# Performance work log

Measured on AMD Instinct MI355X. Metric: run time of the kernel, lower is better.

Reference implementation:

```python
import jax, jax.numpy as jnp
import numpy as np

NUM_HEADS = 16
HEAD_DIM = 128
ROTARY_DIM = 32  # head_dim * rotary_pct(0.25)
ROPE_BASE = 10000.0
SCALE = HEAD_DIM ** -0.5


def _rotate_half(x):
    x1, x2 = jnp.split(x, 2, axis=-1)
    return jnp.concatenate((-x2, x1), axis=-1)


def _rope_tables(seq_len, dtype):
    inv_freq = 1.0 / (ROPE_BASE ** (jnp.arange(0, ROTARY_DIM, 2, dtype=jnp.float32) / ROTARY_DIM))
    freqs = jnp.arange(seq_len, dtype=jnp.float32)[:, None] * inv_freq[None, :]  # [S, rd/2]
    emb = jnp.concatenate((freqs, freqs), axis=-1)  # [S, rd]
    return jnp.cos(emb).astype(dtype), jnp.sin(emb).astype(dtype)


def setup_inputs() -> dict:
    key = jax.random.key(0)
    k1, k2, k3 = jax.random.split(key, 3)
    B, S, H = 2, 2048, 2048
    hidden_states = jax.random.normal(k1, (B, S, H), dtype=jnp.float32)
    attention_mask = jnp.zeros((B, 1, S, S), dtype=jnp.float32)
    Wqkv = jax.random.normal(k2, (H, 3 * H), dtype=jnp.float32) * (H ** -0.5)
    Wout = jax.random.normal(k3, (H, H), dtype=jnp.float32) * (H ** -0.5)
    return {"hidden_states": hidden_states, "attention_mask": attention_mask,
            "Wqkv": Wqkv, "Wout": Wout}


def reference(hidden_states, attention_mask, Wqkv, Wout):
    B, S, H = hidden_states.shape
    qkv = jnp.einsum('bsh,hk->bsk', hidden_states, Wqkv)  # [B,S,3H]
    q, k, v = jnp.split(qkv, 3, axis=-1)

    def to_heads(x):
        return x.reshape(B, S, NUM_HEADS, HEAD_DIM).transpose(0, 2, 1, 3)  # [B,nh,S,hd]

    q, k, v = to_heads(q), to_heads(k), to_heads(v)

    cos, sin = _rope_tables(S, hidden_states.dtype)  # [S, ROTARY_DIM]
    cos = cos[None, None, :, :]
    sin = sin[None, None, :, :]

    def rope(x):
        xr = x[..., :ROTARY_DIM]
        xr = xr * cos + _rotate_half(xr) * sin
        return jnp.concatenate((xr, x[..., ROTARY_DIM:]), axis=-1)

    q, k = rope(q), rope(k)

    scores = jnp.einsum('bhqd,bhkd->bhqk', q, k) * SCALE + attention_mask
    probs = jax.nn.softmax(scores, axis=-1)  # dropout p=0 -> identity
    ctx = jnp.einsum('bhqk,bhkd->bhqd', probs, v)
    ctx = ctx.transpose(0, 2, 1, 3).reshape(B, S, H)
    return jnp.einsum('bsh,ho->bso', ctx, Wout)
```

## Files before the change

### kernel.cpp

```cpp
#include <hip/hip_runtime.h>

typedef __attribute__((ext_vector_type(4))) float f32x4;
typedef __attribute__((ext_vector_type(8))) short s16x8;
typedef __attribute__((ext_vector_type(4))) unsigned short u16x4;
typedef __attribute__((ext_vector_type(8))) unsigned short u16x8;

#define DEVINL __device__ __forceinline__

constexpr int Bb = 2;
constexpr int Ss = 2048;
constexpr int Hh = 2048;
constexpr int NH = 16;
constexpr int HD = 128;
constexpr float ATT_SCALE = 0.08838834764831845f;
constexpr float CEXP = ATT_SCALE * 1.44269504089f;
constexpr float INV_SCALE = 11.313708498984761f;
constexpr float RAW_THR = 90.50966799f;

DEVINL unsigned short f2bf(float f) {
    unsigned u = __float_as_uint(f);
    u += 0x7FFFu + ((u >> 16) & 1u);
    return (unsigned short)(u >> 16);
}
DEVINL float bf2f(unsigned short h) { return __uint_as_float(((unsigned)h) << 16); }
DEVINL float fexp2(float x) { return __builtin_amdgcn_exp2f(x); }

DEVINL void gl16(const void* g, void* l) {
    __builtin_amdgcn_global_load_lds((const __attribute__((address_space(1))) void*)g,
                                     (__attribute__((address_space(3))) void*)l, 16, 0, 0);
}

__global__ void scan_mask_k(const float* __restrict__ m, int* __restrict__ flag) {
    size_t i = ((size_t)blockIdx.x * 256 + threadIdx.x) * 4;
    f32x4 v = *(const f32x4*)(m + i);
    int any = (v[0] != 0.f) || (v[1] != 0.f) || (v[2] != 0.f) || (v[3] != 0.f);
    if (__any(any)) { if ((threadIdx.x & 63) == 0) atomicOr(flag, 1); }
}

__global__ void convH_k(const float* __restrict__ x, unsigned short* __restrict__ y) {
    size_t i = (size_t)blockIdx.x * 256 + threadIdx.x;
    f32x4 a = *(const f32x4*)(x + i * 8);
    f32x4 b = *(const f32x4*)(x + i * 8 + 4);
    u16x8 o;
    o[0] = f2bf(a[0]); o[1] = f2bf(a[1]); o[2] = f2bf(a[2]); o[3] = f2bf(a[3]);
    o[4] = f2bf(b[0]); o[5] = f2bf(b[1]); o[6] = f2bf(b[2]); o[7] = f2bf(b[3]);
    *(u16x8*)(y + i * 8) = o;
}

__global__ void convT_k(const float* __restrict__ W, unsigned short* __restrict__ Wt,
                        int R, int C) {
    __shared__ float tile[32][33];
    int c0 = blockIdx.x * 32, r0 = blockIdx.y * 32;
    int t = threadIdx.x;
    int rr = t >> 3, cc = (t & 7) * 4;
    f32x4 v = *(const f32x4*)(W + (size_t)(r0 + rr) * C + c0 + cc);
    tile[rr][cc + 0] = v[0]; tile[rr][cc + 1] = v[1];
    tile[rr][cc + 2] = v[2]; tile[rr][cc + 3] = v[3];
    __syncthreads();
    u16x4 o;
    o[0] = f2bf(tile[cc + 0][rr]); o[1] = f2bf(tile[cc + 1][rr]);
    o[2] = f2bf(tile[cc + 2][rr]); o[3] = f2bf(tile[cc + 3][rr]);
    *(u16x4*)(Wt + (size_t)(c0 + rr) * R + r0 + cc) = o;
}

template<int MODE>
__global__ __launch_bounds__(512, 2)
void gemm128x256_k(const unsigned short* __restrict__ A, const unsigned short* __restrict__ Bt,
                   float* __restrict__ Cf, unsigned short* __restrict__ Cb,
                   unsigned short* __restrict__ VtOut,
                   int M, int N, int K, int rm, int rn, int snx) {
    __shared__ char lds[98304];
    int t = threadIdx.x, w = t >> 6, ln = t & 63, lr = ln & 15, lg = ln >> 4;
    int wm = w >> 2, wn = w & 3;
    int f = blockIdx.x;
    int xcd = f & 7, i0 = f >> 3;
    int mb = (xcd / snx) * rm + i0 % rm;
    int nb = (xcd % snx) * rn + i0 / rm;
    int m0 = mb * 128, n0 = nb * 256;
    const char* Ab = (const char*)A;
    const char* Bbp = (const char*)Bt;

    f32x4 acc[4][4];
#pragma unroll
    for (int i = 0; i < 4; ++i)
#pragma unroll
        for (int j = 0; j < 4; ++j) { acc[i][j][0] = 0.f; acc[i][j][1] = 0.f; acc[i][j][2] = 0.f; acc[i][j][3] = 0.f; }

    auto STGA = [&](int sbuf, int skh, int kt) {
        int row = t >> 2, c = t & 3;
        int cs = c ^ ((row >> 1) & 3);
        gl16(Ab + ((size_t)(m0 + row) * K + kt * 64 + skh * 32) * 2 + cs * 16,
             lds + sbuf * 49152 + skh * 8192 + t * 16);
    };
    auto STGB = [&](int sbuf, int skh, int kt) {
#pragma unroll
        for (int rr = 0; rr < 2; ++rr) {
            int ci = rr * 512 + t;
            int row = ci >> 2, c = ci & 3;
            int cs = c ^ ((row >> 1) & 3);
            gl16(Bbp + ((size_t)(n0 + row) * K + kt * 64 + skh * 32) * 2 + cs * 16,
                 lds + sbuf * 49152 + 16384 + skh * 16384 + ci * 16);
        }
    };

#define PH128(buf, kh, sbuf, skh, st)                                             \
  {                                                                               \
    const char* Ap = lds + (buf) * 49152 + (kh) * 8192;                           \
    const char* Bp = lds + (buf) * 49152 + 16384 + (kh) * 16384;                  \
    s16x8 af[4], bfr[4];                                                          \
    _Pragma("unroll")                                                             \
    for (int i = 0; i < 4; ++i) {                                                 \
      int row = wm * 64 + i * 16 + lr;                                            \
      af[i] = *(const s16x8*)(Ap + row * 64 + ((lg ^ ((row >> 1) & 3)) * 16));    \
    }                                                                             \
    _Pragma("unroll")                                                             \
    for (int j = 0; j < 4; ++j) {                                                 \
      int row = wn * 64 + j * 16 + lr;                                            \
      bfr[j] = *(const s16x8*)(Bp + row * 64 + ((lg ^ ((row >> 1) & 3)) * 16));   \
    }                                                                             \
    STGA(sbuf, skh, st); STGB(sbuf, skh, st);                                     \
    __builtin_amdgcn_s_barrier();                                                 \
    asm volatile("s_waitcnt lgkmcnt(0)" ::: "memory");                            \
    __builtin_amdgcn_s_setprio(1);                                                \
    _Pragma("unroll")                                                             \
    for (int i = 0; i < 4; ++i)                                                   \
      _Pragma("unroll")                                                           \
      for (int j = 0; j < 4; ++j)                                                 \
        acc[i][j] = __builtin_amdgcn_mfma_f32_16x16x32_bf16(af[i], bfr[j],        \
                                                            acc[i][j], 0, 0, 0); \
    __builtin_amdgcn_s_setprio(0);                                                \
    asm volatile("s_waitcnt vmcnt(6)" ::: "memory");                              \
    __builtin_amdgcn_s_barrier();                                                 \
  }

    const int NT = K >> 6;
    STGA(0, 0, 0); STGB(0, 0, 0);
    STGA(0, 1, 0); STGB(0, 1, 0);
    STGA(1, 0, 1); STGB(1, 0, 1);
    asm volatile("s_waitcnt vmcnt(3)" ::: "memory");
    __builtin_amdgcn_s_barrier();

    for (int it = 0; it < (NT >> 1); ++it) {
        int e = it * 2;
        int e2 = (e + 2 < NT) ? e + 2 : e;
        int e3 = (e + 3 < NT) ? e + 3 : e + 1;
        PH128(0, 0,  1, 1, e + 1)
        PH128(0, 1,  0, 0, e2)
        PH128(1, 0,  0, 1, e2)
        PH128(1, 1,  1, 0, e3)
    }
    asm volatile("s_waitcnt vmcnt(0)" ::: "memory");
#undef PH128

    if (MODE == 0 && n0 >= 4096) {
#pragma unroll
        for (int i = 0; i < 4; ++i)
#pragma unroll
            for (int j = 0; j < 4; ++j) {
                int vcol = n0 - 4096 + wn * 64 + j * 16 + lr;
                int h = vcol >> 7, d = vcol & 127;
                int gr = m0 + wm * 64 + i * 16 + lg * 4;
                int bb = gr >> 11, si = gr & 2047;
                u16x4 o;
                o[0] = f2bf(acc[i][j][0]); o[1] = f2bf(acc[i][j][1]);
                o[2] = f2bf(acc[i][j][2]); o[3] = f2bf(acc[i][j][3]);
                *(u16x4*)(VtOut + ((size_t)(bb * 16 + h) * 128 + d) * 2048 + si) = o;
            }
        return;
    }

    if (MODE == 0 && (wn & 1) == 0) {
        float invf = fexp2((float)lr * -0.83048202372f);
#pragma unroll
        for (int i = 0; i < 4; ++i)
#pragma unroll
            for (int r = 0; r < 4; ++r) {
                int srow = (m0 + wm * 64 + i * 16 + lg * 4 + r) & (Ss - 1);
                float sn, cs;
                sincosf((float)srow * invf, &sn, &cs);
                float x1 = acc[i][0][r], x2 = acc[i][1][r];
                acc[i][0][r] = x1 * cs - x2 * sn;
                acc[i][1][r] = x2 * cs + x1 * sn;
            }
    }

#pragma unroll
    for (int i = 0; i < 4; ++i)
#pragma unroll
        for (int j = 0; j < 4; ++j)
#pragma unroll
            for (int r = 0; r < 4; ++r) {
                int gr = m0 + wm * 64 + i * 16 + lg * 4 + r;
                int gc = n0 + wn * 64 + j * 16 + lr;
                float vv = acc[i][j][r];
                if (MODE == 1) Cf[(size_t)gr * N + gc] = vv;
                else           Cb[(size_t)gr * N + gc] = f2bf(vv);
            }
}

__global__ __launch_bounds__(512)
void attn_k(const unsigned short* __restrict__ qkv, const unsigned short* __restrict__ Vt,
            const float* __restrict__ mask, unsigned short* __restrict__ ctxb,
            const int* __restrict__ flag) {
    __shared__ char ldsK[2][16384];
    __shared__ char ldsV[2][16384];
    __shared__ unsigned short ldsP[8][1024];
    int f = blockIdx.x;
    int swzb = (f & 7) * 64 + (f >> 3);
    int bh = swzb >> 4, qt = swzb & 15;
    int b = bh >> 4, h = bh & 15;
    int t = threadIdx.x, w = t >> 6, ln = t & 63, lr = ln & 15, lg = ln >> 4;
    int useMask = *flag;
    int qw0 = qt * 128 + w * 16;
    const char* qkvB = (const char*)qkv;
    const char* VtB = (const char*)Vt;

    auto STAGE = [&](int buf, int kk0s) {
#pragma unroll
        for (int c = 0; c < 2; ++c) {
            int ci = c * 512 + t;
            int krow = ci >> 4, kcb = (ci & 15) << 4;
            gl16(qkvB + (((size_t)(b * Ss + kk0s + krow)) * 6144 + 2048 + h * 128) * 2 + (kcb ^ ((krow & 7) << 4)),
                 ldsK[buf] + ci * 16);
            int vrow = ci >> 3, vcb = (ci & 7) << 4;
            gl16(VtB + (((size_t)(bh * 128 + vrow)) * 2048 + kk0s) * 2 + (vcb ^ ((vrow & 7) << 4)),
                 ldsV[buf] + ci * 16);
        }
    };

    s16x8 qf[4];
    size_t qbase = ((size_t)(b * Ss + qw0 + lr)) * 6144 + h * 128;
#pragma unroll
    for (int kc = 0; kc < 4; ++kc) qf[kc] = *(const s16x8*)(qkv + qbase + kc * 32 + lg * 8);

    float mr = -3e38f, lsum = 0.f;
    f32x4 ctxa[8];
#pragma unroll
    for (int dn = 0; dn < 8; ++dn) { ctxa[dn][0] = 0.f; ctxa[dn][1] = 0.f; ctxa[dn][2] = 0.f; ctxa[dn][3] = 0.f; }
    const float* mrow = mask + (size_t)b * Ss * Ss;

    STAGE(0, 0);
    asm volatile("s_waitcnt vmcnt(0)" ::: "memory");
    __builtin_amdgcn_s_barrier();

    for (int tix = 0; tix < 32; ++tix) {
        int kk0 = tix * 64;
        int cur = tix & 1;
        if (kk0 + 64 < Ss) STAGE(cur ^ 1, kk0 + 64);

        f32x4 st[4];
#pragma unroll
        for (int n = 0; n < 4; ++n) {
            f32x4 sacc = {0.f, 0.f, 0.f, 0.f};
            const char* kb = ldsK[cur] + (n * 16 + lr) * 256;
            int sw = (lr & 7) << 4;
            s16x8 kf0 = *(const s16x8*)(kb + ((0 * 64 + lg * 16) ^ sw));
            s16x8 kf1 = *(const s16x8*)(kb + ((1 * 64 + lg * 16) ^ sw));
            s16x8 kf2 = *(const s16x8*)(kb + ((2 * 64 + lg * 16) ^ sw));
            s16x8 kf3 = *(const s16x8*)(kb + ((3 * 64 + lg * 16) ^ sw));
            __builtin_amdgcn_s_setprio(1);
            sacc = __builtin_amdgcn_mfma_f32_16x16x32_bf16(kf0, qf[0], sacc, 0, 0, 0);
            sacc = __builtin_amdgcn_mfma_f32_16x16x32_bf16(kf1, qf[1], sacc, 0, 0, 0);
            sacc = __builtin_amdgcn_mfma_f32_16x16x32_bf16(kf2, qf[2], sacc, 0, 0, 0);
            sacc = __builtin_amdgcn_mfma_f32_16x16x32_bf16(kf3, qf[3], sacc, 0, 0, 0);
            __builtin_amdgcn_s_setprio(0);
            st[n] = sacc;
        }
        if (useMask) {
#pragma unroll
            for (int n = 0; n < 4; ++n)
#pragma unroll
                for (int r = 0; r < 4; ++r)
                    st[n][r] += mrow[(size_t)(qw0 + lr) * Ss + kk0 + n * 16 + lg * 4 + r] * INV_SCALE;
        }
        float pmax = st[0][0];
#pragma unroll
        for (int n = 0; n < 4; ++n)
#pragma unroll
            for (int r = 0; r < 4; ++r) pmax = fmaxf(pmax, st[n][r]);
        pmax = fmaxf(pmax, __shfl_xor(pmax, 16));
        pmax = fmaxf(pmax, __shfl_xor(pmax, 32));
        bool need = pmax > mr + RAW_THR;
        if (__any(need)) {
            float mn = fmaxf(mr, pmax);
            float al = fexp2((mr - mn) * CEXP);
            mr = mn;
            lsum *= al;
            float a0 = __shfl(al, lg * 4 + 0), a1 = __shfl(al, lg * 4 + 1);
            float a2 = __shfl(al, lg * 4 + 2), a3 = __shfl(al, lg * 4 + 3);
#pragma unroll
            for (int dn = 0; dn < 8; ++dn) {
                ctxa[dn][0] *= a0; ctxa[dn][1] *= a1; ctxa[dn][2] *= a2; ctxa[dn][3] *= a3;
            }
        }
        float mC = mr * CEXP;
        float rs = 0.f;
        u16x4 pk[4];
#pragma unroll
        for (int n = 0; n < 4; ++n)
#pragma unroll
            for (int r = 0; r < 4; ++r) {
                float p = fexp2(st[n][r] * CEXP - mC);
                rs += p;
                pk[n][r] = f2bf(p);
            }
        rs += __shfl_xor(rs, 16);
        rs += __shfl_xor(rs, 32);
        lsum += rs;
        char* pw = (char*)ldsP[w];
        int swp = (lr & 7) << 4;
#pragma unroll
        for (int n = 0; n < 4; ++n)
            *(u16x4*)(pw + lr * 128 + ((32 * n + 8 * lg) ^ swp)) = pk[n];
        asm volatile("s_waitcnt lgkmcnt(0)" ::: "memory");
        s16x8 pa[2];
#pragma unroll
        for (int c2 = 0; c2 < 2; ++c2)
            pa[c2] = *(const s16x8*)(pw + lr * 128 + ((64 * c2 + 16 * lg) ^ swp));
#pragma unroll
        for (int dn = 0; dn < 8; ++dn) {
            const char* vb = ldsV[cur] + (dn * 16 + lr) * 128;
            s16x8 vf0 = *(const s16x8*)(vb + ((0 * 64 + lg * 16) ^ swp));
            s16x8 vf1 = *(const s16x8*)(vb + ((1 * 64 + lg * 16) ^ swp));
            __builtin_amdgcn_s_setprio(1);
            ctxa[dn] = __builtin_amdgcn_mfma_f32_16x16x32_bf16(pa[0], vf0, ctxa[dn], 0, 0, 0);
            ctxa[dn] = __builtin_amdgcn_mfma_f32_16x16x32_bf16(pa[1], vf1, ctxa[dn], 0, 0, 0);
            __builtin_amdgcn_s_setprio(0);
        }
        asm volatile("s_waitcnt vmcnt(0)" ::: "memory");
        __builtin_amdgcn_s_barrier();
    }
    float l0 = 1.f / __shfl(lsum, lg * 4 + 0), l1 = 1.f / __shfl(lsum, lg * 4 + 1);
    float l2 = 1.f / __shfl(lsum, lg * 4 + 2), l3 = 1.f / __shfl(lsum, lg * 4 + 3);
#pragma unroll
    for (int dn = 0; dn < 8; ++dn) {
        size_t base = ((size_t)(b * Ss + qw0)) * Hh + h * 128 + dn * 16 + lr;
        ctxb[base + (size_t)(lg * 4 + 0) * Hh] = f2bf(ctxa[dn][0] * l0);
        ctxb[base + (size_t)(lg * 4 + 1) * Hh] = f2bf(ctxa[dn][1] * l1);
        ctxb[base + (size_t)(lg * 4 + 2) * Hh] = f2bf(ctxa[dn][2] * l2);
        ctxb[base + (size_t)(lg * 4 + 3) * Hh] = f2bf(ctxa[dn][3] * l3);
    }
}

extern "C" void kernel_launch(void* const* d_in, const int* in_sizes, int n_in,
                              void* d_out, int out_size, void* d_ws, size_t ws_size,
                              hipStream_t stream) {
    (void)in_sizes; (void)n_in; (void)out_size; (void)ws_size;
    const float* hidden = (const float*)d_in[0];
    const float* mask   = (const float*)d_in[1];
    const float* Wqkv   = (const float*)d_in[2];
    const float* Wout   = (const float*)d_in[3];
    float* out = (float*)d_out;

    char* ws = (char*)d_ws;
    size_t off = 0;
    auto alloc = [&](size_t bytes) { char* p = ws + off; off += (bytes + 255) & ~(size_t)255; return p; };
    unsigned short* hbf   = (unsigned short*)alloc((size_t)8388608 * 2);
    unsigned short* wqkvT = (unsigned short*)alloc((size_t)12582912 * 2);
    unsigned short* woutT = (unsigned short*)alloc((size_t)4194304 * 2);
    unsigned short* qkv   = (unsigned short*)alloc((size_t)25165824 * 2);
    unsigned short* Vt    = (unsigned short*)alloc((size_t)8388608 * 2);
    int* flag             = (int*)alloc(256);
    unsigned short* ctx = hbf;

    hipMemsetAsync(flag, 0, 4, stream);
    scan_mask_k<<<8192, 256, 0, stream>>>(mask, flag);
    convH_k<<<4096, 256, 0, stream>>>(hidden, hbf);
    convT_k<<<dim3(192, 64), 256, 0, stream>>>(Wqkv, wqkvT, 2048, 6144);
    convT_k<<<dim3(64, 64), 256, 0, stream>>>(Wout, woutT, 2048, 2048);
    gemm128x256_k<0><<<768, 512, 0, stream>>>(hbf, wqkvT, nullptr, qkv, Vt,
                                              4096, 6144, 2048, 16, 6, 4);
    attn_k<<<512, 512, 0, stream>>>(qkv, Vt, mask, ctx, flag);
    gemm128x256_k<1><<<256, 512, 0, stream>>>(ctx, woutT, out, nullptr, nullptr,
                                              4096, 2048, 2048, 16, 2, 4);
}
```

Before: 300.8 us.

## Rewrite attention kernel with 32x32 MFMA tiles and 4-wave blocks

The attention kernel switches from 16x16x32 to 32x32x16 bf16 MFMA, with each wave owning 32 query rows. Blocks go from 8 waves to 4, with launch bounds allowing 3 blocks per CU. K/V staging drops from double-buffered prefetch to a single buffer loaded synchronously each iteration. Larger MFMA tiles raise data reuse per LDS fragment load and cut shuffle work in softmax, but the loss of prefetch overlap may expose global load latency.

After: 416.5 us. 38.5% more time.

```diff
diff --git a/kernel.cpp b/kernel.cpp
--- a/kernel.cpp
+++ b/kernel.cpp
@@ -1,6 +1,7 @@
 #include <hip/hip_runtime.h>
 
 typedef __attribute__((ext_vector_type(4))) float f32x4;
+typedef __attribute__((ext_vector_type(16))) float f32x16;
 typedef __attribute__((ext_vector_type(8))) short s16x8;
 typedef __attribute__((ext_vector_type(4))) unsigned short u16x4;
 typedef __attribute__((ext_vector_type(8))) unsigned short u16x8;
@@ -198,87 +199,88 @@
             }
 }
 
-__global__ __launch_bounds__(512)
+__global__ __launch_bounds__(256, 3)
 void attn_k(const unsigned short* __restrict__ qkv, const unsigned short* __restrict__ Vt,
             const float* __restrict__ mask, unsigned short* __restrict__ ctxb,
             const int* __restrict__ flag) {
-    __shared__ char ldsK[2][16384];
-    __shared__ char ldsV[2][16384];
-    __shared__ unsigned short ldsP[8][1024];
+    __shared__ char ldsK[16384];
+    __shared__ char ldsV[16384];
+    __shared__ unsigned short ldsP[4][2048];
     int f = blockIdx.x;
     int swzb = (f & 7) * 64 + (f >> 3);
     int bh = swzb >> 4, qt = swzb & 15;
     int b = bh >> 4, h = bh & 15;
-    int t = threadIdx.x, w = t >> 6, ln = t & 63, lr = ln & 15, lg = ln >> 4;
+    int t = threadIdx.x, w = t >> 6, ln = t & 63;
+    int q5 = ln & 31, lg5 = ln >> 5;
     int useMask = *flag;
-    int qw0 = qt * 128 + w * 16;
+    int qb = qt * 128 + w * 32;
     const char* qkvB = (const char*)qkv;
     const char* VtB = (const char*)Vt;
 
-    auto STAGE = [&](int buf, int kk0s) {
-#pragma unroll
-        for (int c = 0; c < 2; ++c) {
-            int ci = c * 512 + t;
-            int krow = ci >> 4, kcb = (ci & 15) << 4;
-            gl16(qkvB + (((size_t)(b * Ss + kk0s + krow)) * 6144 + 2048 + h * 128) * 2 + (kcb ^ ((krow & 7) << 4)),
-                 ldsK[buf] + ci * 16);
-            int vrow = ci >> 3, vcb = (ci & 7) << 4;
-            gl16(VtB + (((size_t)(bh * 128 + vrow)) * 2048 + kk0s) * 2 + (vcb ^ ((vrow & 7) << 4)),
-                 ldsV[buf] + ci * 16);
-        }
-    };
-
-    s16x8 qf[4];
-    size_t qbase = ((size_t)(b * Ss + qw0 + lr)) * 6144 + h * 128;
-#pragma unroll
-    for (int kc = 0; kc < 4; ++kc) qf[kc] = *(const s16x8*)(qkv + qbase + kc * 32 + lg * 8);
+    s16x8 qf[8];
+    size_t qrow = ((size_t)(b * Ss + qb + q5)) * 6144 + h * 128;
+#pragma unroll
+    for (int dc = 0; dc < 8; ++dc) qf[dc] = *(const s16x8*)(qkv + qrow + dc * 16 + lg5 * 8);
 
     float mr = -3e38f, lsum = 0.f;
-    f32x4 ctxa[8];
-#pragma unroll
-    for (int dn = 0; dn < 8; ++dn) { ctxa[dn][0] = 0.f; ctxa[dn][1] = 0.f; ctxa[dn][2] = 0.f; ctxa[dn][3] = 0.f; }
+    f32x16 ctx[4];
+#pragma unroll
+    for (int dt = 0; dt < 4; ++dt)
+#pragma unroll
+        for (int r = 0; r < 16; ++r) ctx[dt][r] = 0.f;
     const float* mrow = mask + (size_t)b * Ss * Ss;
-
-    STAGE(0, 0);
-    asm volatile("s_waitcnt vmcnt(0)" ::: "memory");
-    __builtin_amdgcn_s_barrier();
 
     for (int tix = 0; tix < 32; ++tix) {
         int kk0 = tix * 64;
-        int cur = tix & 1;
-        if (kk0 + 64 < Ss) STAGE(cur ^ 1, kk0 + 64);
-
-        f32x4 st[4];
-#pragma unroll
-        for (int n = 0; n < 4; ++n) {
-            f32x4 sacc = {0.f, 0.f, 0.f, 0.f};
-            const char* kb = ldsK[cur] + (n * 16 + lr) * 256;
-            int sw = (lr & 7) << 4;
-            s16x8 kf0 = *(const s16x8*)(kb + ((0 * 64 + lg * 16) ^ sw));
-            s16x8 kf1 = *(const s16x8*)(kb + ((1 * 64 + lg * 16) ^ sw));
-            s16x8 kf2 = *(const s16x8*)(kb + ((2 * 64 + lg * 16) ^ sw));
-            s16x8 kf3 = *(const s16x8*)(kb + ((3 * 64 + lg * 16) ^ sw));
+#pragma unroll
+        for (int c = 0; c < 4; ++c) {
+            int ci = c * 256 + t;
+            int krow = ci >> 4, kcb = (ci & 15) << 4;
+            gl16(qkvB + (((size_t)(b * Ss + kk0 + krow)) * 6144 + 2048 + h * 128) * 2 + (kcb ^ ((krow & 7) << 4)),
+                 ldsK + ci * 16);
+        }
+#pragma unroll
+        for (int c = 0; c < 4; ++c) {
+            int ci = c * 256 + t;
+            int vrow = ci >> 3, vcb = (ci & 7) << 4;
+            gl16(VtB + (((size_t)(bh * 128 + vrow)) * 2048 + kk0) * 2 + (vcb ^ ((vrow & 7) << 4)),
+                 ldsV + ci * 16);
+        }
+        asm volatile("s_waitcnt vmcnt(0)" ::: "memory");
+        __builtin_amdgcn_s_barrier();
+
+        f32x16 st[2];
+#pragma unroll
+        for (int n = 0; n < 2; ++n) {
+            f32x16 sacc;
+#pragma unroll
+            for (int r = 0; r < 16; ++r) sacc[r] = 0.f;
+            int krow = n * 32 + q5;
+            const char* kb = ldsK + krow * 256;
+            int sw = krow & 7;
             __builtin_amdgcn_s_setprio(1);
-            sacc = __builtin_amdgcn_mfma_f32_16x16x32_bf16(kf0, qf[0], sacc, 0, 0, 0);
-            sacc = __builtin_amdgcn_mfma_f32_16x16x32_bf16(kf1, qf[1], sacc, 0, 0, 0);
-            sacc = __builtin_amdgcn_mfma_f32_16x16x32_bf16(kf2, qf[2], sacc, 0, 0, 0);
-            sacc = __builtin_amdgcn_mfma_f32_16x16x32_bf16(kf3, qf[3], sacc, 0, 0, 0);
+#pragma unroll
+            for (int dc = 0; dc < 8; ++dc) {
+                s16x8 kf = *(const s16x8*)(kb + (((dc * 2 + lg5) ^ sw) << 4));
+                sacc = __builtin_amdgcn_mfma_f32_32x32x16_bf16(kf, qf[dc], sacc, 0, 0, 0);
+            }
             __builtin_amdgcn_s_setprio(0);
             st[n] = sacc;
         }
         if (useMask) {
 #pragma unroll
-            for (int n = 0; n < 4; ++n)
-#pragma unroll
-                for (int r = 0; r < 4; ++r)
-                    st[n][r] += mrow[(size_t)(qw0 + lr) * Ss + kk0 + n * 16 + lg * 4 + r] * INV_SCALE;
+            for (int n = 0; n < 2; ++n)
+#pragma unroll
+                for (int r = 0; r < 16; ++r) {
+                    int kk = n * 32 + (r & 3) + 8 * (r >> 2) + 4 * lg5;
+                    st[n][r] += mrow[(size_t)(qb + q5) * Ss + kk0 + kk] * INV_SCALE;
+                }
         }
         float pmax = st[0][0];
 #pragma unroll
-        for (int n = 0; n < 4; ++n)
-#pragma unroll
-            for (int r = 0; r < 4; ++r) pmax = fmaxf(pmax, st[n][r]);
-        pmax = fmaxf(pmax, __shfl_xor(pmax, 16));
+        for (int n = 0; n < 2; ++n)
+#pragma unroll
+            for (int r = 0; r < 16; ++r) pmax = fmaxf(pmax, st[n][r]);
         pmax = fmaxf(pmax, __shfl_xor(pmax, 32));
         bool need = pmax > mr + RAW_THR;
         if (__any(need)) {
@@ -286,59 +288,63 @@
             float al = fexp2((mr - mn) * CEXP);
             mr = mn;
             lsum *= al;
-            float a0 = __shfl(al, lg * 4 + 0), a1 = __shfl(al, lg * 4 + 1);
-            float a2 = __shfl(al, lg * 4 + 2), a3 = __shfl(al, lg * 4 + 3);
-#pragma unroll
-            for (int dn = 0; dn < 8; ++dn) {
-                ctxa[dn][0] *= a0; ctxa[dn][1] *= a1; ctxa[dn][2] *= a2; ctxa[dn][3] *= a3;
-            }
+#pragma unroll
+            for (int dt = 0; dt < 4; ++dt)
+#pragma unroll
+                for (int r = 0; r < 16; ++r)
+                    ctx[dt][r] *= __shfl(al, (r & 3) + 8 * (r >> 2) + 4 * lg5);
         }
         float mC = mr * CEXP;
         float rs = 0.f;
-        u16x4 pk[4];
-#pragma unroll
-        for (int n = 0; n < 4; ++n)
-#pragma unroll
-            for (int r = 0; r < 4; ++r) {
+#pragma unroll
+        for (int n = 0; n < 2; ++n)
+#pragma unroll
+            for (int r = 0; r < 16; ++r) {
                 float p = fexp2(st[n][r] * CEXP - mC);
                 rs += p;
-                pk[n][r] = f2bf(p);
-            }
-        rs += __shfl_xor(rs, 16);
+                st[n][r] = p;
+            }
         rs += __shfl_xor(rs, 32);
         lsum += rs;
         char* pw = (char*)ldsP[w];
-        int swp = (lr & 7) << 4;
-#pragma unroll
-        for (int n = 0; n < 4; ++n)
-            *(u16x4*)(pw + lr * 128 + ((32 * n + 8 * lg) ^ swp)) = pk[n];
+        int swq = q5 & 7;
+#pragma unroll
+        for (int n = 0; n < 2; ++n)
+#pragma unroll
+            for (int g = 0; g < 4; ++g) {
+                u16x4 o;
+                o[0] = f2bf(st[n][g * 4 + 0]); o[1] = f2bf(st[n][g * 4 + 1]);
+                o[2] = f2bf(st[n][g * 4 + 2]); o[3] = f2bf(st[n][g * 4 + 3]);
+                *(u16x4*)(pw + q5 * 128 + (((n * 4 + g) ^ swq) << 4) + lg5 * 8) = o;
+            }
         asm volatile("s_waitcnt lgkmcnt(0)" ::: "memory");
-        s16x8 pa[2];
-#pragma unroll
-        for (int c2 = 0; c2 < 2; ++c2)
-            pa[c2] = *(const s16x8*)(pw + lr * 128 + ((64 * c2 + 16 * lg) ^ swp));
-#pragma unroll
-        for (int dn = 0; dn < 8; ++dn) {
-            const char* vb = ldsV[cur] + (dn * 16 + lr) * 128;
-            s16x8 vf0 = *(const s16x8*)(vb + ((0 * 64 + lg * 16) ^ swp));
-            s16x8 vf1 = *(const s16x8*)(vb + ((1 * 64 + lg * 16) ^ swp));
+        s16x8 pa[4];
+#pragma unroll
+        for (int c = 0; c < 4; ++c)
+            pa[c] = *(const s16x8*)(pw + q5 * 128 + (((c * 2 + lg5) ^ swq) << 4));
+#pragma unroll
+        for (int dt = 0; dt < 4; ++dt) {
+            int vrow = dt * 32 + q5;
+            const char* vb = ldsV + vrow * 128;
+            int swv = vrow & 7;
             __builtin_amdgcn_s_setprio(1);
-            ctxa[dn] = __builtin_amdgcn_mfma_f32_16x16x32_bf16(pa[0], vf0, ctxa[dn], 0, 0, 0);
-            ctxa[dn] = __builtin_amdgcn_mfma_f32_16x16x32_bf16(pa[1], vf1, ctxa[dn], 0, 0, 0);
+#pragma unroll
+            for (int c = 0; c < 4; ++c) {
+                s16x8 vf = *(const s16x8*)(vb + (((c * 2 + lg5) ^ swv) << 4));
+                ctx[dt] = __builtin_amdgcn_mfma_f32_32x32x16_bf16(pa[c], vf, ctx[dt], 0, 0, 0);
+            }
             __builtin_amdgcn_s_setprio(0);
         }
-        asm volatile("s_waitcnt vmcnt(0)" ::: "memory");
         __builtin_amdgcn_s_barrier();
     }
-    float l0 = 1.f / __shfl(lsum, lg * 4 + 0), l1 = 1.f / __shfl(lsum, lg * 4 + 1);
-    float l2 = 1.f / __shfl(lsum, lg * 4 + 2), l3 = 1.f / __shfl(lsum, lg * 4 + 3);
-#pragma unroll
-    for (int dn = 0; dn < 8; ++dn) {
-        size_t base = ((size_t)(b * Ss + qw0)) * Hh + h * 128 + dn * 16 + lr;
-        ctxb[base + (size_t)(lg * 4 + 0) * Hh] = f2bf(ctxa[dn][0] * l0);
-        ctxb[base + (size_t)(lg * 4 + 1) * Hh] = f2bf(ctxa[dn][1] * l1);
-        ctxb[base + (size_t)(lg * 4 + 2) * Hh] = f2bf(ctxa[dn][2] * l2);
-        ctxb[base + (size_t)(lg * 4 + 3) * Hh] = f2bf(ctxa[dn][3] * l3);
+#pragma unroll
+    for (int r = 0; r < 16; ++r) {
+        int qr = (r & 3) + 8 * (r >> 2) + 4 * lg5;
+        float li = 1.f / __shfl(lsum, qr);
+        size_t base = ((size_t)(b * Ss + qb + qr)) * Hh + h * 128 + q5;
+#pragma unroll
+        for (int dt = 0; dt < 4; ++dt)
+            ctxb[base + dt * 32] = f2bf(ctx[dt][r] * li);
     }
 }
 
@@ -370,7 +376,7 @@
     convT_k<<<dim3(64, 64), 256, 0, stream>>>(Wout, woutT, 2048, 2048);
     gemm128x256_k<0><<<768, 512, 0, stream>>>(hbf, wqkvT, nullptr, qkv, Vt,
                                               4096, 6144, 2048, 16, 6, 4);
-    attn_k<<<512, 512, 0, stream>>>(qkv, Vt, mask, ctx, flag);
+    attn_k<<<512, 256, 0, stream>>>(qkv, Vt, mask, ctx, flag);
     gemm128x256_k<1><<<256, 512, 0, stream>>>(ctx, woutT, out, nullptr, nullptr,
                                               4096, 2048, 2048, 16, 2, 4);
 }
```
